# Kernel optimization log

Measured on AMD Instinct MI355X. Metric: run time of the kernel, lower is better.

Reference implementation:

```python
import jax, jax.numpy as jnp
import numpy as np

D = H = W = 64
N = D * H * W
BS = 2
C = 32          # enc_dim
IN_DIM = 4
OUT_DIM = 4
P = 5           # pos_enc_dim
COND = 32
M = 8           # modes per axis
NL = 4          # n_layers
NODE_IN = IN_DIM + 3 + 2 * P * 3   # 37
ENC_T = 1 + 2 * P                  # 11
ENC_C = ENC_T * COND               # 352
DT = 0.05


def fourier_embedding(pos, n_freq):
    # F(x) = [cos(2^i*pi*x_l), sin(2^i*pi*x_l)] per coordinate l, then concat x
    freq = (2.0 ** jnp.arange(n_freq, dtype=jnp.float32)) * jnp.pi  # (P,)
    ang = pos[..., None] * freq                                     # (..., L, P)
    emb = jnp.concatenate([jnp.cos(ang), jnp.sin(ang)], axis=-1)    # (..., L, 2P)
    emb = emb.reshape(*pos.shape[:-1], -1)                          # (..., L*2P)
    return jnp.concatenate([emb, pos], axis=-1)


def setup_inputs() -> dict:
    key = jax.random.key(0)
    ks = jax.random.split(key, 24)
    scale = 1.0 / C ** 2
    inp = {
        "state_in": jax.random.normal(ks[0], (BS, N, IN_DIM), jnp.float32),
        "node_pos": jax.random.uniform(ks[1], (BS, N, 3), jnp.float32),
        "edges": jax.random.randint(ks[2], (BS, 16, 2), 0, N),
        "time_i": jax.random.uniform(ks[3], (BS, 1), jnp.float32),
        "conditions": jax.random.uniform(ks[4], (BS, COND), jnp.float32),
        "t_embed_w": jax.random.normal(ks[5], (C, ENC_T), jnp.float32) * 0.05,
        "t_embed_b": jax.random.normal(ks[6], (C,), jnp.float32) * 0.05,
        "c_embed_w": jax.random.normal(ks[7], (C, ENC_C), jnp.float32) * 0.05,
        "c_embed_b": jax.random.normal(ks[8], (C,), jnp.float32) * 0.05,
        "lift_w": jax.random.normal(ks[9], (C, NODE_IN), jnp.float32) * 0.05,
        "lift_b": jax.random.normal(ks[10], (C,), jnp.float32) * 0.05,
        "spec_wr": jax.random.uniform(ks[11], (NL, C, C, M, M, M), jnp.float32) * scale,
        "spec_wi": jax.random.uniform(ks[12], (NL, C, C, M, M, M), jnp.float32) * scale,
        "byp_w": jax.random.normal(ks[13], (NL, C, C), jnp.float32) * 0.05,
        "byp_b": jax.random.normal(ks[14], (NL, C), jnp.float32) * 0.05,
        "proj1_w": jax.random.normal(ks[15], (C, C), jnp.float32) * 0.05,
        "proj1_b": jax.random.normal(ks[16], (C,), jnp.float32) * 0.05,
        "proj2_w": jax.random.normal(ks[17], (OUT_DIM, C), jnp.float32) * 0.05,
        "proj2_b": jax.random.normal(ks[18], (OUT_DIM,), jnp.float32) * 0.05,
    }
    return inp


def _conv1x1(x, w, b):
    # x: (b, c, d, h, w), w: (o, c), b: (o,)
    return jnp.einsum('bcdhw,oc->bodhw', x, w) + b[None, :, None, None, None]


def _fno_forward(state_in, node_pos, time_i, conditions,
                 t_embed_w, t_embed_b, c_embed_w, c_embed_b, lift_w, lift_b,
                 spec_wr, spec_wi, byp_w, byp_b, proj1_w, proj1_b, proj2_w, proj2_b):
    pos_enc = fourier_embedding(node_pos, P)      # (bs, N, 33)
    c_enc = fourier_embedding(conditions, P)      # (bs, 352)
    t_enc = fourier_embedding(time_i, P)          # (bs, 11)

    node_feat = jnp.concatenate([state_in, pos_enc], axis=-1)  # (bs, N, 37)
    t_emb = (t_enc @ t_embed_w.T + t_embed_b)[:, :, None, None, None]
    c_emb = (c_enc @ c_embed_w.T + c_embed_b)[:, :, None, None, None]

    # (bs, N, 37) -> (bs, 37, D, H, W)
    x = node_feat.transpose(0, 2, 1).reshape(BS, NODE_IN, D, H, W)
    x = _conv1x1(x, lift_w, lift_b)
    x = x + t_emb + c_emb

    for l in range(NL):
        w = jax.lax.complex(spec_wr[l], spec_wi[l])              # (C, C, M, M, M)
        x_ft = jnp.fft.rfftn(x, axes=(-3, -2, -1))               # (bs, C, D, H, W//2+1)
        blk = jnp.einsum('bixyz,ioxyz->boxyz', x_ft[..., :M, :M, :M], w)
        out_ft = jnp.zeros_like(x_ft).at[..., :M, :M, :M].set(blk)
        sp = jnp.fft.irfftn(out_ft, s=(D, H, W), axes=(-3, -2, -1))
        bp = _conv1x1(x, byp_w[l], byp_b[l])
        x = jax.nn.gelu(sp + bp, approximate=False)

    x = jax.nn.gelu(_conv1x1(x, proj1_w, proj1_b), approximate=False)
    x = _conv1x1(x, proj2_w, proj2_b)                            # (bs, 4, D, H, W)
    v_pred = x.reshape(BS, OUT_DIM, N).transpose(0, 2, 1)        # (bs, N, 4)
    return state_in + DT * v_pred


def reference(state_in, node_pos, edges, time_i, conditions,
              t_embed_w, t_embed_b, c_embed_w, c_embed_b, lift_w, lift_b,
              spec_wr, spec_wi, byp_w, byp_b, proj1_w, proj1_b, proj2_w, proj2_b):
    # edges are unused in the FNO forward (kept for API compatibility)
    return _fno_forward(state_in, node_pos, time_i, conditions,
                        t_embed_w, t_embed_b, c_embed_w, c_embed_b, lift_w, lift_b,
                        spec_wr, spec_wi, byp_w, byp_b, proj1_w, proj1_b, proj2_w, proj2_b)
```

## Files before the change

kernel.cpp:

```cpp
#include <hip/hip_runtime.h>
#include <math.h>

#define PI_F 3.14159265358979323846f

typedef __bf16 bf16x8 __attribute__((ext_vector_type(8)));
typedef float floatx4 __attribute__((ext_vector_type(4)));
union U8 { unsigned short u[8]; uint4 q; bf16x8 v; };

__device__ __forceinline__ float gelu_sig(float v) {
    float e = __builtin_amdgcn_exp2f(-2.4554670f * v);
    return v * __builtin_amdgcn_rcpf(1.0f + e);
}
__device__ __forceinline__ int rfl(int x) { return __builtin_amdgcn_readfirstlane(x); }

__device__ __forceinline__ unsigned short f2bf(float f) {
    unsigned int u = __float_as_uint(f);
    u += 0x7fffu + ((u >> 16) & 1u);
    return (unsigned short)(u >> 16);
}
__device__ __forceinline__ float bf2f(unsigned short h) {
    return __uint_as_float(((unsigned int)h) << 16);
}
__device__ __forceinline__ unsigned int pack2(float a, float b) {
    return (unsigned int)f2bf(a) | ((unsigned int)f2bf(b) << 16);
}

__global__ void k_wt(const float* __restrict__ time_i, const float* __restrict__ conditions,
                     const float* __restrict__ t_embed_w, const float* __restrict__ t_embed_b,
                     const float* __restrict__ c_embed_w, const float* __restrict__ c_embed_b,
                     const float* __restrict__ lift_b, float* __restrict__ embk,
                     const float* __restrict__ byp_w, const float* __restrict__ lift_w,
                     unsigned short* __restrict__ wbh, unsigned short* __restrict__ wlbf,
                     unsigned short* __restrict__ Tinv, unsigned short* __restrict__ TfT,
                     float* __restrict__ Tp1g, const float* __restrict__ spec_wr,
                     const float* __restrict__ spec_wi, float2* __restrict__ wT) {
    const float th = PI_F / 32.0f;
    __shared__ float red[8][32];
    __shared__ __align__(16) float2 TT[4160];
    int t = threadIdx.x;
    if (blockIdx.x < 2) {
        int b = blockIdx.x;
        int c = t & 31, lg = t >> 5;
        float acc = 0.0f;
        if (lg == 0) {
            acc = t_embed_b[c] + c_embed_b[c] + lift_b[c];
            float tv = time_i[b];
            float ang = PI_F * tv;
            const float* tw = t_embed_w + c * 11;
            for (int i = 0; i < 5; i++) {
                float s, co; sincosf(ang, &s, &co);
                acc += co * tw[i] + s * tw[5 + i];
                ang *= 2.0f;
            }
            acc += tv * tw[10];
        }
        const float* cw = c_embed_w + c * 352;
        for (int j = 0; j < 4; j++) {
            int l = lg * 4 + j;
            float v = conditions[b * 32 + l];
            float ang = PI_F * v;
            for (int i = 0; i < 5; i++) {
                float s, co; sincosf(ang, &s, &co);
                acc += co * cw[l * 10 + i] + s * cw[l * 10 + 5 + i];
                ang *= 2.0f;
            }
            acc += v * cw[320 + l];
        }
        red[lg][c] = acc;
        __syncthreads();
        if (t < 32) {
            float s = 0.0f;
            for (int g = 0; g < 8; g++) s += red[g][t];
            embk[b * 32 + t] = s;
        }
        return;
    }
    if (blockIdx.x >= 40) {
        int n = blockIdx.x - 40;
        int l = n >> 7, i = (n & 127) >> 2, og = n & 3;
        size_t srcb = ((size_t)(l * 1024 + i * 32 + og * 8)) * 512;
        for (int k = 0; k < 16; k++) {
            int e = k * 256 + t;
            TT[(e >> 9) * 520 + (e & 511)] =
                make_float2(spec_wr[srcb + e], spec_wi[srcb + e]);
        }
        __syncthreads();
        for (int k = 0; k < 16; k++) {
            int e = k * 256 + t;
            int o = e & 7, mo = e >> 3;
            int sm = ((mo & 7) << 6) | (mo & 56) | (mo >> 6);
            wT[(size_t)l * 524288 + (size_t)mo * 1024 + i * 32 + og * 8 + o]
                = TT[o * 520 + sm];
        }
        return;
    }
    int idx = (blockIdx.x - 2) * 256 + t;
    if (idx < 4096) {
        wbh[idx] = f2bf(byp_w[idx]);
    } else if (idx < 6144) {
        int j = idx - 4096;
        int o = j >> 6, q = j & 63;
        wlbf[j] = (q < 37) ? f2bf(lift_w[o * 37 + q]) : 0;
    } else if (idx < 8192) {
        int j = idx - 6144;
        int nz = j >> 5, k = j & 31;
        int kz = k >> 1;
        float val = 0.0f;
        if (kz < 8) {
            float a = (float)((kz * nz) & 63) * th;
            val = (k & 1) ? sinf(a) : cosf(a);
            val *= (kz == 0) ? (1.0f / 262144.0f) : (2.0f / 262144.0f);
        }
        Tinv[j] = f2bf(val);
    } else if (idx < 9216) {
        int j = idx - 8192;
        int kcol = j >> 6, nz = j & 63;
        int kz = kcol >> 1;
        float a = (float)((kz * nz) & 63) * th;
        float val = (kcol & 1) ? -sinf(a) : cosf(a);
        TfT[j] = f2bf(val);
    } else if (idx < 9728) {
        int j = idx - 9216;
        int ny = j >> 3, ky = j & 7;
        float a = (float)((ky * ny) & 63) * th;
        Tp1g[j * 2] = cosf(a);
        Tp1g[j * 2 + 1] = sinf(a);
    }
}

__device__ __forceinline__ void swz8k(int blk, int& b, int& nx, int& ny) {
    int x = blk & 7;
    int j = blk >> 3;
    int pair = x * 16 + (j >> 6);
    ny = j & 63;
    b = pair >> 6;
    nx = pair & 63;
}


__global__ __launch_bounds__(256) void k_lift(const float* __restrict__ state_in,
        const float* __restrict__ node_pos, const unsigned short* __restrict__ wlbf,
        const float* __restrict__ embk, const unsigned short* __restrict__ TfT,
        unsigned short* __restrict__ x0, unsigned int* __restrict__ a1) {
    __shared__ __align__(16) float SL[3456];
    unsigned short* fsT  = (unsigned short*)SL;
    unsigned short* ysbf = (unsigned short*)(SL + 2304);
    int t = threadIdx.x;
    int b, nx, ny; swz8k(blockIdx.x, b, nx, ny);
    int nxy = nx * 64 + ny;

    {
        for (int u = t; u < 2048; u += 256) {
            int row = u >> 5, col = 37 + (u & 31);
            fsT[row * 72 + col] = 0;
        }
    }
    if (t < 192) {
        int nzf = t / 3;
        int l = t - nzf * 3;
        float p = node_pos[((size_t)b * 262144 + (nxy << 6)) * 3 + t];
        float s, c; sincosf(PI_F * p, &s, &c);
        unsigned short* row = fsT + nzf * 72;
        #pragma unroll
        for (int i = 0; i < 5; i++) {
            row[4 + l * 10 + i] = f2bf(c);
            row[4 + l * 10 + 5 + i] = f2bf(s);
            float nc = 2.0f * c * c - 1.0f;
            s = 2.0f * s * c;
            c = nc;
        }
        row[34 + l] = f2bf(p);
    } else {
        int nzf = t - 192;
        const float4 s4 = *(const float4*)(state_in + ((size_t)b * 262144 + (nxy << 6) + nzf) * 4);
        unsigned short* row = fsT + nzf * 72;
        row[0] = f2bf(s4.x); row[1] = f2bf(s4.y);
        row[2] = f2bf(s4.z); row[3] = f2bf(s4.w);
    }
    __syncthreads();

    int lane = t & 63;
    int w = rfl(t >> 6);
    int l15 = lane & 15;
    int quad = lane >> 4;
    int nz = w * 16 + l15;
    size_t xbase = ((size_t)(b * 4096 + nxy)) * 2048;

    U8 b0, b1_;
    b0.q  = *(const uint4*)(fsT + nz * 72 + (quad << 3));
    b1_.q = *(const uint4*)(fsT + nz * 72 + 32 + (quad << 3));
    unsigned short hh[2][4];
    #pragma unroll
    for (int ot = 0; ot < 2; ot++) {
        U8 aA, aB;
        aA.q = *(const uint4*)(wlbf + ((ot * 16 + l15) << 6) + (quad << 3));
        aB.q = *(const uint4*)(wlbf + ((ot * 16 + l15) << 6) + 32 + (quad << 3));
        float4 cbv = *(const float4*)(embk + b * 32 + ot * 16 + quad * 4);
        floatx4 cb = {cbv.x, cbv.y, cbv.z, cbv.w};
        floatx4 d = __builtin_amdgcn_mfma_f32_16x16x32_bf16(aA.v, b0.v, cb, 0, 0, 0);
        d = __builtin_amdgcn_mfma_f32_16x16x32_bf16(aB.v, b1_.v, d, 0, 0, 0);
        #pragma unroll
        for (int r = 0; r < 4; r++) {
            hh[ot][r] = f2bf(d[r]);
            ysbf[(ot * 16 + quad * 4 + r) * 72 + nz] = hh[ot][r];
        }
    }
    *(uint4*)(x0 + xbase + nz * 32 + (quad << 3)) = make_uint4(
        (unsigned)hh[0][0] | ((unsigned)hh[0][1] << 16),
        (unsigned)hh[0][2] | ((unsigned)hh[0][3] << 16),
        (unsigned)hh[1][0] | ((unsigned)hh[1][1] << 16),
        (unsigned)hh[1][2] | ((unsigned)hh[1][3] << 16));
    __syncthreads();

    if (w < 2) {
        int o = w * 16 + l15;
        U8 ay0, ay1, bt0, bt1;
        ay0.q = *(const uint4*)(ysbf + o * 72 + (quad << 3));
        ay1.q = *(const uint4*)(ysbf + o * 72 + 32 + (quad << 3));
        bt0.q = *(const uint4*)(TfT + (l15 << 6) + (quad << 3));
        bt1.q = *(const uint4*)(TfT + (l15 << 6) + 32 + (quad << 3));
        floatx4 z = {0.0f, 0.0f, 0.0f, 0.0f};
        z = __builtin_amdgcn_mfma_f32_16x16x32_bf16(ay0.v, bt0.v, z, 0, 0, 0);
        z = __builtin_amdgcn_mfma_f32_16x16x32_bf16(ay1.v, bt1.v, z, 0, 0, 0);
        float p0 = __shfl_xor(z[0], 1), p1 = __shfl_xor(z[1], 1);
        float p2 = __shfl_xor(z[2], 1), p3 = __shfl_xor(z[3], 1);
        if (!(lane & 1)) {
            unsigned int* a1p = a1 + ((size_t)(b * 4096 + nxy)) * 256;
            int kz = l15 >> 1;
            a1p[(w * 16 + quad * 4 + 0) * 8 + kz] = pack2(z[0], p0);
            a1p[(w * 16 + quad * 4 + 1) * 8 + kz] = pack2(z[1], p1);
            a1p[(w * 16 + quad * 4 + 2) * 8 + kz] = pack2(z[2], p2);
            a1p[(w * 16 + quad * 4 + 3) * 8 + kz] = pack2(z[3], p3);
        }
    }
}


__global__ __launch_bounds__(256) void k_ps1(const unsigned int* __restrict__ a1,
        const float2* __restrict__ Tp1g, float2* __restrict__ a2p) {
    int blk = blockIdx.x, t = threadIdx.x;
    int x = blk & 7, r = blk >> 3;
    int pair = x * 16 + (r & 15);
    int qtr = r >> 4;
    const unsigned int* src = a1 + ((size_t)(pair * 64 + qtr * 16)) * 256 + t;
    float accr[8], acci[8];
    #pragma unroll
    for (int k = 0; k < 8; k++) { accr[k] = 0.0f; acci[k] = 0.0f; }
    #pragma unroll 4
    for (int j = 0; j < 16; j++) {
        int ny = qtr * 16 + j;
        unsigned int pv = src[(size_t)j * 256];
        float vx = bf2f((unsigned short)(pv & 0xffffu));
        float vy = bf2f((unsigned short)(pv >> 16));
        const float2* tw = Tp1g + ny * 8;
        #pragma unroll
        for (int ky = 0; ky < 8; ky++) {
            float2 w2 = tw[ky];
            accr[ky] += vx * w2.x + vy * w2.y;
            acci[ky] += vy * w2.x - vx * w2.y;
        }
    }
    int b = pair >> 6, nx = pair & 63;
    int c = t >> 3, kz = t & 7;
    float2* dst = a2p + ((size_t)((qtr * 2 + b) * 8 + kz)) * 16384 + nx * 32 + c;
    #pragma unroll
    for (int ky = 0; ky < 8; ky++)
        dst[(size_t)ky * 2048] = make_float2(accr[ky], acci[ky]);
}

__global__ __launch_bounds__(256) void k_ps2(const float2* __restrict__ a2p,
        const float2* __restrict__ wTl, const float2* __restrict__ Tp1g,
        float2* __restrict__ b1) {
    __shared__ __align__(16) float2 MS[2048];
    __shared__ __align__(16) float2 TW[512];
    __shared__ __align__(16) float2 XS[256];
    __shared__ __align__(16) float2 YS[288];
    int t = threadIdx.x, blk = blockIdx.x;
    int b = blk >> 6, kz = (blk >> 3) & 7, ky = blk & 7;
    size_t sb = (size_t)b * 131072 + kz * 16384 + ky * 2048;
    for (int k = 0; k < 8; k++) {
        int e = k * 256 + t;
        float2 v0 = a2p[sb + e];
        float2 v1 = a2p[sb + 262144 + e];
        float2 v2 = a2p[sb + 524288 + e];
        float2 v3 = a2p[sb + 786432 + e];
        MS[e] = make_float2(v0.x + v1.x + v2.x + v3.x,
                            v0.y + v1.y + v2.y + v3.y);
    }
    TW[t] = Tp1g[t];
    TW[256 + t] = Tp1g[256 + t];
    __syncthreads();
    {
        int c = t >> 3, kx = t & 7;
        float xr = 0.0f, xi = 0.0f;
        #pragma unroll 8
        for (int nx = 0; nx < 64; nx++) {
            float2 v = MS[nx * 32 + c];
            float2 w2 = TW[nx * 8 + kx];
            xr += v.x * w2.x + v.y * w2.y;
            xi += v.y * w2.x - v.x * w2.y;
        }
        XS[c * 8 + kx] = make_float2(xr, xi);
    }
    __syncthreads();
    {
        int kx = t >> 5, o = t & 31;
        const float2* wp = wTl + ((size_t)(kz * 64 + ky * 8 + kx)) * 1024 + o;
        float yr = 0.0f, yi = 0.0f;
        #pragma unroll 8
        for (int i = 0; i < 32; i++) {
            float2 xv = XS[i * 8 + kx];
            float2 wv = wp[i * 32];
            yr += xv.x * wv.x - xv.y * wv.y;
            yi += xv.x * wv.y + xv.y * wv.x;
        }
        YS[o * 9 + kx] = make_float2(yr, yi);
    }
    __syncthreads();
    {
        int nx8 = t >> 5, o = t & 31;
        for (int j = 0; j < 8; j++) {
            int nx = nx8 * 8 + j;
            float rr = 0.0f, ri = 0.0f;
            #pragma unroll
            for (int kx = 0; kx < 8; kx++) {
                float2 y = YS[o * 9 + kx];
                float2 w2 = TW[nx * 8 + kx];
                rr += y.x * w2.x - y.y * w2.y;
                ri += y.x * w2.y + y.y * w2.x;
            }
            b1[((size_t)(b * 64 + nx)) * 2048 + (kz * 8 + ky) * 32 + o]
                = make_float2(rr, ri);
        }
    }
}

__global__ __launch_bounds__(256) void k_fin(
        const unsigned short* __restrict__ xin, const float2* __restrict__ b1,
        const unsigned short* __restrict__ wbh, const float* __restrict__ bb,
        const unsigned short* __restrict__ Tinv, const unsigned short* __restrict__ TfT,
        const float2* __restrict__ Tp1g, unsigned short* __restrict__ xout,
        unsigned int* __restrict__ a1, int do_z, int do_proj,
        const float* __restrict__ state_in, const float* __restrict__ p1w,
        const float* __restrict__ p1b, const float* __restrict__ p2w,
        const float* __restrict__ p2b, float* __restrict__ outp) {
    __shared__ __align__(16) float S[5632];
    float* bstage = S;
    float* pr = S;
    unsigned int* msu = (unsigned int*)(S + 4224);
    unsigned short* ysbf = (unsigned short*)(S + 4480);
    int t = threadIdx.x;
    int b, nx, ny; swz8k(blockIdx.x, b, nx, ny);
    int nxy = nx * 64 + ny;
    int lane = t & 63;
    int w = rfl(t >> 6);
    int l15 = lane & 15;
    int quad = lane >> 4;
    int nz = w * 16 + l15;
    size_t xbase = ((size_t)(b * 4096 + nxy)) * 2048;

    int posA = ((quad & 1) << 4) | ((quad >> 1) << 2);
    uint2 xlo = *(const uint2*)(xin + xbase + nz * 32 + posA);
    uint2 xhi = *(const uint2*)(xin + xbase + nz * 32 + posA + 8);
    U8 bx, btv, aw0, aw1;
    ((uint2*)&bx)[0] = xlo; ((uint2*)&bx)[1] = xhi;
    btv.q = *(const uint4*)(Tinv + (nz << 5) + (quad << 3));
    aw0.q = *(const uint4*)(wbh + (l15 << 5) + (quad << 3));
    aw1.q = *(const uint4*)(wbh + ((16 + l15) << 5) + (quad << 3));
    float4 c0 = *(const float4*)(bb + quad * 4);
    float4 c1 = *(const float4*)(bb + 16 + quad * 4);
    floatx4 cb0 = {c0.x, c0.y, c0.z, c0.w};
    floatx4 cb1 = {c1.x, c1.y, c1.z, c1.w};

    {
        const float4* b1g = (const float4*)(b1 + ((size_t)(b * 64 + nx)) * 2048);
        #pragma unroll
        for (int j = 0; j < 4; j++) {
            int p = j * 256 + t;
            float4 v = b1g[p];
            int s = p * 2;
            *(float4*)((char*)bstage + s * 8 + ((s >> 6) << 4)) = v;
        }
    }
    __syncthreads();

    {
        int o_ = t >> 3, kz_ = t & 7;
        const float2* tw = Tp1g + ny * 8;
        float mr = 0.0f, mi = 0.0f;
        #pragma unroll
        for (int ky = 0; ky < 8; ky++) {
            int g = kz_ * 256 + ky * 32 + o_;
            float2 v = *(const float2*)((char*)bstage + g * 8 + ((g >> 6) << 4));
            float2 w2 = tw[ky];
            mr += v.x * w2.x - v.y * w2.y;
            mi += v.x * w2.y + v.y * w2.x;
        }
        msu[o_ * 8 + kz_] = pack2(mr, -mi);
    }
    __syncthreads();

    U8 am0, am1;
    if (quad < 2) {
        am0.q = *(const uint4*)(msu + l15 * 8 + quad * 4);
        am1.q = *(const uint4*)(msu + (16 + l15) * 8 + quad * 4);
    } else {
        am0.q = make_uint4(0, 0, 0, 0);
        am1.q = make_uint4(0, 0, 0, 0);
    }
    floatx4 d0 = __builtin_amdgcn_mfma_f32_16x16x32_bf16(aw0.v, bx.v, cb0, 0, 0, 0);
    d0 = __builtin_amdgcn_mfma_f32_16x16x32_bf16(am0.v, btv.v, d0, 0, 0, 0);
    floatx4 d1 = __builtin_amdgcn_mfma_f32_16x16x32_bf16(aw1.v, bx.v, cb1, 0, 0, 0);
    d1 = __builtin_amdgcn_mfma_f32_16x16x32_bf16(am1.v, btv.v, d1, 0, 0, 0);

    unsigned short h0[4], h1[4];
    #pragma unroll
    for (int r = 0; r < 4; r++) {
        h0[r] = f2bf(gelu_sig(d0[r]));
        ysbf[(quad * 4 + r) * 72 + nz] = h0[r];
        h1[r] = f2bf(gelu_sig(d1[r]));
        ysbf[(16 + quad * 4 + r) * 72 + nz] = h1[r];
    }
    if (!do_proj) {
        *(uint4*)(xout + xbase + nz * 32 + (quad << 3)) = make_uint4(
            (unsigned)h0[0] | ((unsigned)h0[1] << 16),
            (unsigned)h0[2] | ((unsigned)h0[3] << 16),
            (unsigned)h1[0] | ((unsigned)h1[1] << 16),
            (unsigned)h1[2] | ((unsigned)h1[3] << 16));
    }
    __syncthreads();

    if (do_z && w < 2) {
        int o = w * 16 + l15;
        U8 ay0, ay1, bt0, bt1;
        ay0.q = *(const uint4*)(ysbf + o * 72 + (quad << 3));
        ay1.q = *(const uint4*)(ysbf + o * 72 + 32 + (quad << 3));
        bt0.q = *(const uint4*)(TfT + (l15 << 6) + (quad << 3));
        bt1.q = *(const uint4*)(TfT + (l15 << 6) + 32 + (quad << 3));
        floatx4 z = {0.0f, 0.0f, 0.0f, 0.0f};
        z = __builtin_amdgcn_mfma_f32_16x16x32_bf16(ay0.v, bt0.v, z, 0, 0, 0);
        z = __builtin_amdgcn_mfma_f32_16x16x32_bf16(ay1.v, bt1.v, z, 0, 0, 0);
        float p0 = __shfl_xor(z[0], 1), p1 = __shfl_xor(z[1], 1);
        float p2 = __shfl_xor(z[2], 1), p3 = __shfl_xor(z[3], 1);
        if (!(lane & 1)) {
            unsigned int* a1p = a1 + ((size_t)(b * 4096 + nxy)) * 256;
            int kz = l15 >> 1;
            a1p[(w * 16 + quad * 4 + 0) * 8 + kz] = pack2(z[0], p0);
            a1p[(w * 16 + quad * 4 + 1) * 8 + kz] = pack2(z[1], p1);
            a1p[(w * 16 + quad * 4 + 2) * 8 + kz] = pack2(z[2], p2);
            a1p[(w * 16 + quad * 4 + 3) * 8 + kz] = pack2(z[3], p3);
        }
    }

    if (do_proj) {
        int nzp = t & 63;
        float xv[32];
        #pragma unroll
        for (int i = 0; i < 32; i++) xv[i] = bf2f(ysbf[i * 72 + nzp]);
        float r0 = 0.f, r1 = 0.f, r2 = 0.f, r3 = 0.f;
        #pragma unroll
        for (int k = 0; k < 8; k++) {
            int o = w * 8 + k;
            float a = p1b[o];
            const float* wr = p1w + o * 32;
            #pragma unroll
            for (int i = 0; i < 32; i++) a += wr[i] * xv[i];
            float h = gelu_sig(a);
            r0 += p2w[0 * 32 + o] * h;
            r1 += p2w[1 * 32 + o] * h;
            r2 += p2w[2 * 32 + o] * h;
            r3 += p2w[3 * 32 + o] * h;
        }
        *(float4*)(pr + w * 256 + nzp * 4) = make_float4(r0, r1, r2, r3);
        __syncthreads();
        if (t < 64) {
            float4 a0 = *(float4*)(pr + 0 * 256 + t * 4);
            float4 a1_ = *(float4*)(pr + 1 * 256 + t * 4);
            float4 a2 = *(float4*)(pr + 2 * 256 + t * 4);
            float4 a3 = *(float4*)(pr + 3 * 256 + t * 4);
            size_t base = ((size_t)b * 262144 + (nxy << 6) + t) * 4;
            float4 sv = *(const float4*)(state_in + base);
            *(float4*)(outp + base) = make_float4(
                sv.x + 0.05f * (p2b[0] + a0.x + a1_.x + a2.x + a3.x),
                sv.y + 0.05f * (p2b[1] + a0.y + a1_.y + a2.y + a3.y),
                sv.z + 0.05f * (p2b[2] + a0.z + a1_.z + a2.z + a3.z),
                sv.w + 0.05f * (p2b[3] + a0.w + a1_.w + a2.w + a3.w));
        }
    }
}

extern "C" void kernel_launch(void* const* d_in, const int* in_sizes, int n_in,
                              void* d_out, int out_size, void* d_ws, size_t ws_size,
                              hipStream_t stream) {
    const float* state_in   = (const float*)d_in[0];
    const float* node_pos   = (const float*)d_in[1];
    const float* time_i     = (const float*)d_in[3];
    const float* conditions = (const float*)d_in[4];
    const float* t_embed_w  = (const float*)d_in[5];
    const float* t_embed_b  = (const float*)d_in[6];
    const float* c_embed_w  = (const float*)d_in[7];
    const float* c_embed_b  = (const float*)d_in[8];
    const float* lift_w     = (const float*)d_in[9];
    const float* lift_b     = (const float*)d_in[10];
    const float* spec_wr    = (const float*)d_in[11];
    const float* spec_wi    = (const float*)d_in[12];
    const float* byp_w      = (const float*)d_in[13];
    const float* byp_b      = (const float*)d_in[14];
    const float* proj1_w    = (const float*)d_in[15];
    const float* proj1_b    = (const float*)d_in[16];
    const float* proj2_w    = (const float*)d_in[17];
    const float* proj2_b    = (const float*)d_in[18];
    float* out = (float*)d_out;
    float* ws  = (float*)d_ws;

    unsigned short* xA = (unsigned short*)ws;
    unsigned short* xB = (unsigned short*)(ws + 8388608);
    unsigned int* a1 = (unsigned int*)(ws + 16777216);
    float2* a2p  = (float2*)(ws + 20971520);
    float2* b1   = (float2*)(ws + 23396352);
    float*  embk = ws + 23920640;
    unsigned short* wbh  = (unsigned short*)(ws + 23920704);
    unsigned short* wlbf = (unsigned short*)(ws + 23922752);
    unsigned short* Tinv = (unsigned short*)(ws + 23923776);
    unsigned short* TfT  = (unsigned short*)(ws + 23924800);
    float* Tp1gf = ws + 23925312;
    float2* Tp1g = (float2*)Tp1gf;
    float2* wT   = (float2*)(ws + 23926336);

    k_wt<<<552, 256, 0, stream>>>(time_i, conditions, t_embed_w, t_embed_b,
                                  c_embed_w, c_embed_b, lift_b, embk,
                                  byp_w, lift_w, wbh, wlbf, Tinv, TfT, Tp1gf,
                                  spec_wr, spec_wi, wT);
    k_lift<<<8192, 256, 0, stream>>>(state_in, node_pos, wlbf, embk, TfT, xA, a1);

    for (int l = 0; l < 4; l++) {
        unsigned short* xin  = (l & 1) ? xB : xA;
        unsigned short* xout = (l & 1) ? xA : xB;
        k_ps1<<<512, 256, 0, stream>>>(a1, Tp1g, a2p);
        k_ps2<<<128, 256, 0, stream>>>(a2p, wT + (size_t)l * 524288, Tp1g, b1);
        k_fin<<<8192, 256, 0, stream>>>(xin, b1, wbh + l * 1024, byp_b + l * 32,
                                        Tinv, TfT, Tp1g, xout, a1, (l < 3) ? 1 : 0,
                                        (l == 3) ? 1 : 0, state_in,
                                        proj1_w, proj1_b, proj2_w, proj2_b, out);
    }
}
```

Baseline: 308.4 us.

## Fuse ny-DFT partial sum into spectral mid kernel with kz-major a1 layout

Removes the separate k_ps1 kernel and the a2p partial-sum buffer by computing the ny-axis DFT inside the mid kernel for each (b,kz,ky) block. The a1 intermediate is reorganised to a kz-major layout so the lift/fin kernels write it with single 16-byte stores and k_mid reads contiguous channel vectors. This saves one launch and a global round-trip per layer. In exchange, each of the 8 ky blocks re-reads the same (b,kz) slice of a1, and the fused stage runs on only 128 blocks.

```diff
diff --git a/kernel.cpp b/kernel.cpp
--- a/kernel.cpp
+++ b/kernel.cpp
@@ -225,77 +225,59 @@
         float p0 = __shfl_xor(z[0], 1), p1 = __shfl_xor(z[1], 1);
         float p2 = __shfl_xor(z[2], 1), p3 = __shfl_xor(z[3], 1);
         if (!(lane & 1)) {
-            unsigned int* a1p = a1 + ((size_t)(b * 4096 + nxy)) * 256;
             int kz = l15 >> 1;
-            a1p[(w * 16 + quad * 4 + 0) * 8 + kz] = pack2(z[0], p0);
-            a1p[(w * 16 + quad * 4 + 1) * 8 + kz] = pack2(z[1], p1);
-            a1p[(w * 16 + quad * 4 + 2) * 8 + kz] = pack2(z[2], p2);
-            a1p[(w * 16 + quad * 4 + 3) * 8 + kz] = pack2(z[3], p3);
-        }
-    }
-}
-
-
-__global__ __launch_bounds__(256) void k_ps1(const unsigned int* __restrict__ a1,
-        const float2* __restrict__ Tp1g, float2* __restrict__ a2p) {
-    int blk = blockIdx.x, t = threadIdx.x;
-    int x = blk & 7, r = blk >> 3;
-    int pair = x * 16 + (r & 15);
-    int qtr = r >> 4;
-    const unsigned int* src = a1 + ((size_t)(pair * 64 + qtr * 16)) * 256 + t;
-    float accr[8], acci[8];
-    #pragma unroll
-    for (int k = 0; k < 8; k++) { accr[k] = 0.0f; acci[k] = 0.0f; }
-    #pragma unroll 4
-    for (int j = 0; j < 16; j++) {
-        int ny = qtr * 16 + j;
-        unsigned int pv = src[(size_t)j * 256];
-        float vx = bf2f((unsigned short)(pv & 0xffffu));
-        float vy = bf2f((unsigned short)(pv >> 16));
-        const float2* tw = Tp1g + ny * 8;
-        #pragma unroll
-        for (int ky = 0; ky < 8; ky++) {
-            float2 w2 = tw[ky];
-            accr[ky] += vx * w2.x + vy * w2.y;
-            acci[ky] += vy * w2.x - vx * w2.y;
-        }
-    }
-    int b = pair >> 6, nx = pair & 63;
-    int c = t >> 3, kz = t & 7;
-    float2* dst = a2p + ((size_t)((qtr * 2 + b) * 8 + kz)) * 16384 + nx * 32 + c;
-    #pragma unroll
-    for (int ky = 0; ky < 8; ky++)
-        dst[(size_t)ky * 2048] = make_float2(accr[ky], acci[ky]);
-}
-
-__global__ __launch_bounds__(256) void k_ps2(const float2* __restrict__ a2p,
+            unsigned int* a1p = a1 + ((size_t)((b * 8 + kz) * 4096 + nxy)) * 32
+                                + w * 16 + quad * 4;
+            *(uint4*)a1p = make_uint4(pack2(z[0], p0), pack2(z[1], p1),
+                                      pack2(z[2], p2), pack2(z[3], p3));
+        }
+    }
+}
+
+
+__global__ __launch_bounds__(256) void k_mid(const unsigned int* __restrict__ a1,
         const float2* __restrict__ wTl, const float2* __restrict__ Tp1g,
         float2* __restrict__ b1) {
-    __shared__ __align__(16) float2 MS[2048];
+    __shared__ __align__(16) float2 YS1[2112];
     __shared__ __align__(16) float2 TW[512];
     __shared__ __align__(16) float2 XS[256];
     __shared__ __align__(16) float2 YS[288];
     int t = threadIdx.x, blk = blockIdx.x;
     int b = blk >> 6, kz = (blk >> 3) & 7, ky = blk & 7;
-    size_t sb = (size_t)b * 131072 + kz * 16384 + ky * 2048;
-    for (int k = 0; k < 8; k++) {
-        int e = k * 256 + t;
-        float2 v0 = a2p[sb + e];
-        float2 v1 = a2p[sb + 262144 + e];
-        float2 v2 = a2p[sb + 524288 + e];
-        float2 v3 = a2p[sb + 786432 + e];
-        MS[e] = make_float2(v0.x + v1.x + v2.x + v3.x,
-                            v0.y + v1.y + v2.y + v3.y);
-    }
     TW[t] = Tp1g[t];
     TW[256 + t] = Tp1g[256 + t];
+    {
+        int nx = t >> 2, cg = t & 3;
+        const unsigned int* src = a1 + ((size_t)(b * 8 + kz)) * 131072
+                                  + (size_t)nx * 2048 + cg * 8;
+        float ar[8], ai[8];
+        #pragma unroll
+        for (int c = 0; c < 8; c++) { ar[c] = 0.0f; ai[c] = 0.0f; }
+        #pragma unroll 4
+        for (int ny = 0; ny < 64; ny++) {
+            uint4 v0 = *(const uint4*)(src + ny * 32);
+            uint4 v1 = *(const uint4*)(src + ny * 32 + 4);
+            float2 w2 = Tp1g[ny * 8 + ky];
+            unsigned int pv[8] = {v0.x, v0.y, v0.z, v0.w, v1.x, v1.y, v1.z, v1.w};
+            #pragma unroll
+            for (int c = 0; c < 8; c++) {
+                float vx = bf2f((unsigned short)(pv[c] & 0xffffu));
+                float vy = bf2f((unsigned short)(pv[c] >> 16));
+                ar[c] += vx * w2.x + vy * w2.y;
+                ai[c] += vy * w2.x - vx * w2.y;
+            }
+        }
+        #pragma unroll
+        for (int c = 0; c < 8; c++)
+            YS1[nx * 33 + cg * 8 + c] = make_float2(ar[c], ai[c]);
+    }
     __syncthreads();
     {
         int c = t >> 3, kx = t & 7;
         float xr = 0.0f, xi = 0.0f;
         #pragma unroll 8
         for (int nx = 0; nx < 64; nx++) {
-            float2 v = MS[nx * 32 + c];
+            float2 v = YS1[nx * 33 + c];
             float2 w2 = TW[nx * 8 + kx];
             xr += v.x * w2.x + v.y * w2.y;
             xi += v.y * w2.x - v.x * w2.y;
@@ -443,12 +425,11 @@
         float p0 = __shfl_xor(z[0], 1), p1 = __shfl_xor(z[1], 1);
         float p2 = __shfl_xor(z[2], 1), p3 = __shfl_xor(z[3], 1);
         if (!(lane & 1)) {
-            unsigned int* a1p = a1 + ((size_t)(b * 4096 + nxy)) * 256;
             int kz = l15 >> 1;
-            a1p[(w * 16 + quad * 4 + 0) * 8 + kz] = pack2(z[0], p0);
-            a1p[(w * 16 + quad * 4 + 1) * 8 + kz] = pack2(z[1], p1);
-            a1p[(w * 16 + quad * 4 + 2) * 8 + kz] = pack2(z[2], p2);
-            a1p[(w * 16 + quad * 4 + 3) * 8 + kz] = pack2(z[3], p3);
+            unsigned int* a1p = a1 + ((size_t)((b * 8 + kz) * 4096 + nxy)) * 32
+                                + w * 16 + quad * 4;
+            *(uint4*)a1p = make_uint4(pack2(z[0], p0), pack2(z[1], p1),
+                                      pack2(z[2], p2), pack2(z[3], p3));
         }
     }
 
@@ -516,7 +497,6 @@
     unsigned short* xA = (unsigned short*)ws;
     unsigned short* xB = (unsigned short*)(ws + 8388608);
     unsigned int* a1 = (unsigned int*)(ws + 16777216);
-    float2* a2p  = (float2*)(ws + 20971520);
     float2* b1   = (float2*)(ws + 23396352);
     float*  embk = ws + 23920640;
     unsigned short* wbh  = (unsigned short*)(ws + 23920704);
@@ -536,8 +516,7 @@
     for (int l = 0; l < 4; l++) {
         unsigned short* xin  = (l & 1) ? xB : xA;
         unsigned short* xout = (l & 1) ? xA : xB;
-        k_ps1<<<512, 256, 0, stream>>>(a1, Tp1g, a2p);
-        k_ps2<<<128, 256, 0, stream>>>(a2p, wT + (size_t)l * 524288, Tp1g, b1);
+        k_mid<<<128, 256, 0, stream>>>(a1, wT + (size_t)l * 524288, Tp1g, b1);
         k_fin<<<8192, 256, 0, stream>>>(xin, b1, wbh + l * 1024, byp_b + l * 32,
                                         Tinv, TfT, Tp1g, xout, a1, (l < 3) ? 1 : 0,
                                         (l == 3) ? 1 : 0, state_in,
```

Result: slower. 321.0 us (+4.1%).
